# Kernel tuning notes

Measured on AMD Instinct MI355X. Metric: run time of the kernel, lower is better.

Reference implementation:

```python
import jax, jax.numpy as jnp
import numpy as np

B, S, T, E = 16, 512, 128, 256
VIN, VOUT, ENC, DEC = 32000, 32000, 32, 128


def pos_encoding(length, depth):
    # standard sinusoidal positional encoding (TF tutorial / AddPositionalEmbedding)
    half = depth // 2
    pos = jnp.arange(length, dtype=jnp.float32)[:, None]          # (L,1)
    rates = (1.0 / (10000.0 ** (jnp.arange(half, dtype=jnp.float32) / half)))[None, :]
    ang = pos * rates                                             # (L, depth/2)
    return jnp.concatenate([jnp.sin(ang), jnp.cos(ang)], axis=-1)  # (L, depth)


def lstm_scan(x, W, U, b, reverse=False):
    # Keras LSTM, gate order i,f,g,o; zero initial state. x: (B,S,E) -> (B,S,H), h_final
    Bn, H = x.shape[0], U.shape[0]
    def step(carry, xt):
        h, c = carry
        z = xt @ W + h @ U + b
        i, f, g, o = jnp.split(z, 4, axis=-1)
        c = jax.nn.sigmoid(f) * c + jax.nn.sigmoid(i) * jnp.tanh(g)
        h = jax.nn.sigmoid(o) * jnp.tanh(c)
        return (h, c), h
    h0 = jnp.zeros((Bn, H), x.dtype)
    (h, _), hs = jax.lax.scan(step, (h0, h0), jnp.swapaxes(x, 0, 1), reverse=reverse)
    return jnp.swapaxes(hs, 0, 1), h


def setup_inputs() -> dict:
    key = jax.random.key(0)
    ks = jax.random.split(key, 20)
    s = 0.05
    return {
        'source': jax.random.randint(ks[0], (B, S), 0, VIN, dtype=jnp.int32),
        'target': jax.random.randint(ks[1], (B, T), 0, VOUT, dtype=jnp.int32),
        'src_emb': jax.random.normal(ks[2], (VIN, E), jnp.float32) * s,
        'tgt_emb': jax.random.normal(ks[3], (VOUT, E), jnp.float32) * s,
        'Wf': jax.random.normal(ks[4], (E, 4 * ENC), jnp.float32) * s,
        'Uf': jax.random.normal(ks[5], (ENC, 4 * ENC), jnp.float32) * s,
        'bf': jnp.zeros((4 * ENC,), jnp.float32),
        'Wb': jax.random.normal(ks[6], (E, 4 * ENC), jnp.float32) * s,
        'Ub': jax.random.normal(ks[7], (ENC, 4 * ENC), jnp.float32) * s,
        'bb': jnp.zeros((4 * ENC,), jnp.float32),
        'W1': jax.random.normal(ks[8], (2 * ENC, DEC), jnp.float32) * s,
        'b1': jnp.zeros((DEC,), jnp.float32),
        'W2': jax.random.normal(ks[9], (2 * ENC, DEC), jnp.float32) * s,
        'b2': jnp.zeros((DEC,), jnp.float32),
        'Vw': jax.random.normal(ks[10], (DEC, 1), jnp.float32) * s,
        'Vb': jnp.zeros((1,), jnp.float32),
        'Wd': jax.random.normal(ks[11], (2 * ENC + E, 4 * DEC), jnp.float32) * s,
        'bd': jnp.zeros((4 * DEC,), jnp.float32),
        'Wfc': jax.random.normal(ks[12], (DEC, VOUT), jnp.float32) * s,
        'bfc': jnp.zeros((VOUT,), jnp.float32),
    }


def reference(source, target, src_emb, tgt_emb, Wf, Uf, bf, Wb, Ub, bb,
              W1, b1, W2, b2, Vw, Vb, Wd, bd, Wfc, bfc):
    # source embedding + positional encoding
    src = src_emb[source] * jnp.sqrt(jnp.float32(E)) + pos_encoding(S, E)  # (B,S,E)
    # bidirectional encoder (enc_units=32 each direction)
    out_f, hf = lstm_scan(src, Wf, Uf, bf)
    out_b, hb = lstm_scan(src, Wb, Ub, bb, reverse=True)
    enc = jnp.concatenate([out_f, out_b], axis=-1)        # (B,S,64)
    hidden = jnp.concatenate([hf, hb], axis=-1)           # (B,64) — constant query
    # Bahdanau attention with constant query -> constant context vector
    score = jnp.tanh(hidden[:, None, :] @ W1 + b1 + enc @ W2 + b2) @ Vw + Vb  # (B,S,1)
    attw = jax.nn.softmax(score, axis=1)
    ctx = jnp.sum(attw * enc, axis=1)                     # (B,64)
    # per-timestep decoder: LSTM restarts from zero state each step, so all
    # T steps are independent -> vectorize single LSTM step over T
    temb = tgt_emb[target]                                # (B,T,E)
    x = jnp.concatenate(
        [jnp.broadcast_to(ctx[:, None, :], (B, T, 2 * ENC)), temb], axis=-1)  # (B,T,320)
    z = x @ Wd + bd
    i, f, g, o = jnp.split(z, 4, axis=-1)
    c = jax.nn.sigmoid(i) * jnp.tanh(g)                   # c_prev = 0 => forget gate inert
    h = jax.nn.sigmoid(o) * jnp.tanh(c)                   # (B,T,128)
    return h @ Wfc + bfc                                  # (B,T,VOUT)
```

## Files before the change

kernel.cpp:

```cpp
#include <hip/hip_runtime.h>
#include <hip/hip_bf16.h>
#include <math.h>

#define BB 16
#define SS 512
#define TT 128
#define EE 256
#define ENC 32
#define DEC 128
#define VOUT 32000

typedef _Float16 half8 __attribute__((ext_vector_type(8)));
typedef float floatx4 __attribute__((ext_vector_type(4)));

__device__ __forceinline__ float sigmoidf_(float x) { return 1.0f / (1.0f + expf(-x)); }
__device__ __forceinline__ float rcpf_(float x) { return __builtin_amdgcn_rcpf(x); }

__global__ __launch_bounds__(256) void k_embed_gemm(
    const int* __restrict__ source, const float* __restrict__ src_emb,
    const float* __restrict__ Wf, const float* __restrict__ bf,
    const float* __restrict__ Wb, const float* __restrict__ bb,
    float* __restrict__ Zf, float* __restrict__ Zb)
{
    __shared__ __align__(16) float sSrc[8][EE];
    const int r0 = blockIdx.x * 8;
    const int tid = threadIdx.x;

    for (int idx = tid; idx < 8 * EE; idx += 256) {
        const int r = idx >> 8, e = idx & 255;
        const int row = r0 + r;
        const int s = row & (SS - 1);
        const int tok = source[row];
        float v = src_emb[(size_t)tok * EE + e] * 16.0f;
        const int jh = (e < 128) ? e : (e - 128);
        const float rate = expf(-0.07195578415f * (float)jh);
        const float ang = (float)s * rate;
        v += (e < 128) ? sinf(ang) : cosf(ang);
        sSrc[r][e] = v;
    }
    __syncthreads();

    const int j = tid & 127;
    const float* W = (tid < 128) ? Wf : Wb;
    const float* bv = (tid < 128) ? bf : bb;
    float* Zo = (tid < 128) ? Zf : Zb;

    float acc[8];
    const float bias = bv[j];
#pragma unroll
    for (int r = 0; r < 8; ++r) acc[r] = bias;

    for (int e = 0; e < EE; e += 4) {
        const float w0 = W[(e + 0) * 128 + j];
        const float w1 = W[(e + 1) * 128 + j];
        const float w2 = W[(e + 2) * 128 + j];
        const float w3 = W[(e + 3) * 128 + j];
#pragma unroll
        for (int r = 0; r < 8; ++r) {
            const float4 x = *(const float4*)&sSrc[r][e];
            acc[r] = fmaf(x.x, w0, acc[r]);
            acc[r] = fmaf(x.y, w1, acc[r]);
            acc[r] = fmaf(x.z, w2, acc[r]);
            acc[r] = fmaf(x.w, w3, acc[r]);
        }
    }
#pragma unroll
    for (int r = 0; r < 8; ++r) Zo[(size_t)(r0 + r) * 128 + j] = acc[r];
}

__global__ __launch_bounds__(64) void k_scan(
    const float* __restrict__ Zf, const float* __restrict__ Zb,
    const float* __restrict__ Uf, const float* __restrict__ Ub,
    float* __restrict__ enc, float* __restrict__ hidden)
{
    const int blk = blockIdx.x;
    const int batch = blk >> 1;
    const int dir = blk & 1;
    const float* __restrict__ Z = dir ? Zb : Zf;
    const float* __restrict__ U = dir ? Ub : Uf;
    const int lane = threadIdx.x;
    const int u = lane & 31;
    const int half = lane >> 5;
    const int colA = half * 64 + u;
    const int colB = half * 64 + 32 + u;

    float uA[ENC], uB[ENC];
#pragma unroll
    for (int k = 0; k < ENC; ++k) {
        uA[k] = U[k * 128 + colA];
        uB[k] = U[k * 128 + colB];
    }

    const float* __restrict__ Zrow = Z + (size_t)batch * (SS * 128);
    const int dt = dir ? -1 : 1;
    int t = dir ? (SS - 1) : 0;
    float zA = Zrow[t * 128 + colA];
    float zB = Zrow[t * 128 + colB];

    const float m = half ? 2.0f : 1.0f;
    const float madd = 1.0f - m;

    float h = 0.0f, c = 0.0f;

    for (int step = 0; step < SS; ++step) {
        float accA0 = zA, accA1 = 0.f, accA2 = 0.f, accA3 = 0.f;
        float accB0 = zB, accB1 = 0.f, accB2 = 0.f, accB3 = 0.f;
        if (step < SS - 1) {
            const int tn = t + dt;
            zA = Zrow[tn * 128 + colA];
            zB = Zrow[tn * 128 + colB];
        }
#pragma unroll
        for (int k = 0; k < ENC; k += 4) {
            const float h0 = __builtin_bit_cast(float,
                __builtin_amdgcn_readlane(__builtin_bit_cast(int, h), k + 0));
            const float h1 = __builtin_bit_cast(float,
                __builtin_amdgcn_readlane(__builtin_bit_cast(int, h), k + 1));
            const float h2 = __builtin_bit_cast(float,
                __builtin_amdgcn_readlane(__builtin_bit_cast(int, h), k + 2));
            const float h3 = __builtin_bit_cast(float,
                __builtin_amdgcn_readlane(__builtin_bit_cast(int, h), k + 3));
            accA0 = fmaf(h0, uA[k + 0], accA0);
            accB0 = fmaf(h0, uB[k + 0], accB0);
            accA1 = fmaf(h1, uA[k + 1], accA1);
            accB1 = fmaf(h1, uB[k + 1], accB1);
            accA2 = fmaf(h2, uA[k + 2], accA2);
            accB2 = fmaf(h2, uB[k + 2], accB2);
            accA3 = fmaf(h3, uA[k + 3], accA3);
            accB3 = fmaf(h3, uB[k + 3], accB3);
        }
        const float zAv = (accA0 + accA1) + (accA2 + accA3);
        const float zBv = (accB0 + accB1) + (accB2 + accB3);

        const float s1 = rcpf_(1.0f + expf(-m * zAv));
        const float a1 = fmaf(s1, m, madd);
        const float a2 = rcpf_(1.0f + expf(-zBv));

        const float t1 = __shfl_xor(a1, 32);
        const float t2 = __shfl_xor(a2, 32);

        c = fmaf(a2, c, a1 * t1);
        const float e2 = expf(-2.0f * c);
        const float tc = (1.0f - e2) * rcpf_(1.0f + e2);
        h = t2 * tc;

        if (half == 0)
            enc[((size_t)batch * SS + t) * 64 + dir * ENC + u] = h;
        t += dt;
    }
    if (half == 0)
        hidden[batch * 64 + dir * ENC + u] = h;
}

__global__ __launch_bounds__(128) void k_q(
    const float* __restrict__ hidden, const float* __restrict__ W1,
    const float* __restrict__ b1, const float* __restrict__ b2,
    float* __restrict__ q2)
{
    const int b = blockIdx.x, d = threadIdx.x;
    __shared__ __align__(16) float shid[64];
    if (d < 64) shid[d] = hidden[b * 64 + d];
    __syncthreads();
    float acc = b1[d] + b2[d];
#pragma unroll
    for (int k = 0; k < 64; k += 4) {
        const float4 h4 = *(const float4*)&shid[k];
        acc = fmaf(h4.x, W1[(k + 0) * 128 + d], acc);
        acc = fmaf(h4.y, W1[(k + 1) * 128 + d], acc);
        acc = fmaf(h4.z, W1[(k + 2) * 128 + d], acc);
        acc = fmaf(h4.w, W1[(k + 3) * 128 + d], acc);
    }
    q2[b * 128 + d] = acc;
}

__global__ __launch_bounds__(128) void k_score(
    const float* __restrict__ enc, const float* __restrict__ q2,
    const float* __restrict__ W2, const float* __restrict__ Vw,
    const float* __restrict__ Vb, float* __restrict__ scores)
{
    const int bs = blockIdx.x;
    const int b = bs >> 9;
    const int tid = threadIdx.x;
    __shared__ __align__(16) float se[64];
    __shared__ float sred2[2];
    if (tid < 64) se[tid] = enc[(size_t)bs * 64 + tid];
    __syncthreads();
    float acc = q2[b * 128 + tid];
#pragma unroll
    for (int k = 0; k < 64; k += 4) {
        const float4 e4 = *(const float4*)&se[k];
        acc = fmaf(e4.x, W2[(k + 0) * 128 + tid], acc);
        acc = fmaf(e4.y, W2[(k + 1) * 128 + tid], acc);
        acc = fmaf(e4.z, W2[(k + 2) * 128 + tid], acc);
        acc = fmaf(e4.w, W2[(k + 3) * 128 + tid], acc);
    }
    float v = tanhf(acc) * Vw[tid];
#pragma unroll
    for (int off = 32; off > 0; off >>= 1) v += __shfl_down(v, off);
    if ((tid & 63) == 0) sred2[tid >> 6] = v;
    __syncthreads();
    if (tid == 0) scores[bs] = sred2[0] + sred2[1] + Vb[0];
}

__global__ __launch_bounds__(512) void k_softmax_ctx(
    const float* __restrict__ scores, const float* __restrict__ enc,
    float* __restrict__ ctx)
{
    const int b = blockIdx.x, tid = threadIdx.x;
    __shared__ float sw[SS];
    __shared__ float sred[SS];
    const float sc = scores[b * SS + tid];
    sred[tid] = sc;
    __syncthreads();
    for (int s2 = 256; s2 > 0; s2 >>= 1) {
        if (tid < s2) sred[tid] = fmaxf(sred[tid], sred[tid + s2]);
        __syncthreads();
    }
    const float mx = sred[0];
    __syncthreads();
    const float ex = expf(sc - mx);
    sw[tid] = ex;
    sred[tid] = ex;
    __syncthreads();
    for (int s2 = 256; s2 > 0; s2 >>= 1) {
        if (tid < s2) sred[tid] += sred[tid + s2];
        __syncthreads();
    }
    const float inv = 1.0f / sred[0];
    __syncthreads();
    const int d = tid & 63, chunk = tid >> 6;
    float acc = 0.0f;
    const int sbeg = chunk * 64;
    for (int s = sbeg; s < sbeg + 64; ++s)
        acc = fmaf(sw[s], enc[((size_t)b * SS + s) * 64 + d], acc);
    sred[tid] = acc * inv;
    __syncthreads();
    if (tid < 64) {
        float t = 0.0f;
#pragma unroll
        for (int c = 0; c < 8; ++c) t += sred[c * 64 + tid];
        ctx[b * 64 + tid] = t;
    }
}

__global__ __launch_bounds__(384) void k_dec(
    const int* __restrict__ target, const float* __restrict__ tgt_emb,
    const float* __restrict__ ctx, const float* __restrict__ Wd,
    const float* __restrict__ bd, unsigned short* __restrict__ Ah)
{
    const int bt0 = blockIdx.x * 8;
    const int tid = threadIdx.x;
    __shared__ __align__(16) float sx[8][320];
    __shared__ float sg[3][8][128];

    for (int idx = tid; idx < 8 * 320; idx += 384) {
        const int r = idx / 320, k = idx % 320;
        const int bt = bt0 + r;
        const int b = bt >> 7;
        float v;
        if (k < 64) v = ctx[b * 64 + k];
        else v = tgt_emb[(size_t)target[bt] * EE + (k - 64)];
        sx[r][k] = v;
    }
    __syncthreads();

    const int g = tid >> 7, u = tid & 127;
    const int col = (g == 0) ? u : ((g == 1) ? (256 + u) : (384 + u));
    float acc[8];
    const float bias = bd[col];
#pragma unroll
    for (int r = 0; r < 8; ++r) acc[r] = bias;

#pragma unroll 2
    for (int k = 0; k < 320; k += 4) {
        const float w0 = Wd[(k + 0) * 512 + col];
        const float w1 = Wd[(k + 1) * 512 + col];
        const float w2 = Wd[(k + 2) * 512 + col];
        const float w3 = Wd[(k + 3) * 512 + col];
#pragma unroll
        for (int r = 0; r < 8; ++r) {
            const float4 x = *(const float4*)&sx[r][k];
            acc[r] = fmaf(x.x, w0, acc[r]);
            acc[r] = fmaf(x.y, w1, acc[r]);
            acc[r] = fmaf(x.z, w2, acc[r]);
            acc[r] = fmaf(x.w, w3, acc[r]);
        }
    }
#pragma unroll
    for (int r = 0; r < 8; ++r) {
        const float a = acc[r];
        sg[g][r][u] = (g == 1) ? tanhf(a) : sigmoidf_(a);
    }
    __syncthreads();
    if (tid < 128) {
#pragma unroll
        for (int r = 0; r < 8; ++r) {
            const float i_ = sg[0][r][u];
            const float g_ = sg[1][r][u];
            const float o_ = sg[2][r][u];
            const float h = o_ * tanhf(i_ * g_);
            Ah[(size_t)(bt0 + r) * 128 + u] =
                __builtin_bit_cast(unsigned short, (_Float16)h);
        }
    }
}

__global__ __launch_bounds__(256) void k_cvtB(
    const float* __restrict__ Wfc, unsigned short* __restrict__ Bt)
{
    __shared__ __align__(16) unsigned short sH[64][136];
    const int n0 = blockIdx.x * 64;
    const int tid = threadIdx.x;
    const int kk = tid >> 4;
    const int n4 = tid & 15;

#pragma unroll
    for (int p = 0; p < 8; ++p) {
        const int k = p * 16 + kk;
        const float4 v = *(const float4*)&Wfc[(size_t)k * VOUT + n0 + n4 * 4];
        sH[n4 * 4 + 0][k] = __builtin_bit_cast(unsigned short, (_Float16)v.x);
        sH[n4 * 4 + 1][k] = __builtin_bit_cast(unsigned short, (_Float16)v.y);
        sH[n4 * 4 + 2][k] = __builtin_bit_cast(unsigned short, (_Float16)v.z);
        sH[n4 * 4 + 3][k] = __builtin_bit_cast(unsigned short, (_Float16)v.w);
    }
    __syncthreads();

    const int r0 = tid >> 4;
    const int l8 = (tid & 15) * 8;
#pragma unroll
    for (int p = 0; p < 4; ++p) {
        const int r = p * 16 + r0;
        *(uint4*)&Bt[(size_t)(n0 + r) * 128 + l8] = *(const uint4*)&sH[r][l8];
    }
}

__global__ __launch_bounds__(256) void k_out_f16(
    const unsigned short* __restrict__ Ah,
    const unsigned short* __restrict__ Bt,
    const float* __restrict__ bias, float* __restrict__ C)
{
    const int tid  = threadIdx.x;
    const int wave = tid >> 6;
    const int lane = tid & 63;
    const int wm = wave >> 1, wn = wave & 1;
    const int rb = blockIdx.y * 128 + wm * 64;
    const int cb = blockIdx.x * 128 + wn * 64;
    const int lm = lane & 15;
    const int quad = lane >> 4;

    floatx4 acc[4][4];
#pragma unroll
    for (int nt = 0; nt < 4; ++nt) {
        const float bv = bias[cb + nt * 16 + lm];
#pragma unroll
        for (int mt = 0; mt < 4; ++mt)
            acc[mt][nt] = (floatx4){bv, bv, bv, bv};
    }

    const unsigned short* pA = Ah + (size_t)(rb + lm) * 128 + quad * 8;
    const unsigned short* pB = Bt + (size_t)(cb + lm) * 128 + quad * 8;

#pragma unroll
    for (int kc = 0; kc < 128; kc += 32) {
        half8 af[4], bfr[4];
#pragma unroll
        for (int mt = 0; mt < 4; ++mt)
            af[mt] = *(const half8*)(pA + mt * (16 * 128) + kc);
#pragma unroll
        for (int nt = 0; nt < 4; ++nt)
            bfr[nt] = *(const half8*)(pB + nt * (16 * 128) + kc);
#pragma unroll
        for (int mt = 0; mt < 4; ++mt)
#pragma unroll
            for (int nt = 0; nt < 4; ++nt)
                acc[mt][nt] = __builtin_amdgcn_mfma_f32_16x16x32_f16(
                    af[mt], bfr[nt], acc[mt][nt], 0, 0, 0);
    }

#pragma unroll
    for (int mt = 0; mt < 4; ++mt) {
        const int r0 = rb + mt * 16 + quad * 4;
#pragma unroll
        for (int nt = 0; nt < 4; ++nt) {
            const int col = cb + nt * 16 + lm;
            float* Cp = C + (size_t)r0 * VOUT + col;
#pragma unroll
            for (int r = 0; r < 4; ++r)
                Cp[(size_t)r * VOUT] = acc[mt][nt][r];
        }
    }
}

extern "C" void kernel_launch(void* const* d_in, const int* in_sizes, int n_in,
                              void* d_out, int out_size, void* d_ws, size_t ws_size,
                              hipStream_t stream) {
    (void)in_sizes; (void)n_in; (void)out_size; (void)ws_size;
    const int*   source  = (const int*)  d_in[0];
    const int*   target  = (const int*)  d_in[1];
    const float* src_emb = (const float*)d_in[2];
    const float* tgt_emb = (const float*)d_in[3];
    const float* Wf      = (const float*)d_in[4];
    const float* Uf      = (const float*)d_in[5];
    const float* bf      = (const float*)d_in[6];
    const float* Wb      = (const float*)d_in[7];
    const float* Ub      = (const float*)d_in[8];
    const float* bb      = (const float*)d_in[9];
    const float* W1      = (const float*)d_in[10];
    const float* b1      = (const float*)d_in[11];
    const float* W2      = (const float*)d_in[12];
    const float* b2      = (const float*)d_in[13];
    const float* Vw      = (const float*)d_in[14];
    const float* Vb      = (const float*)d_in[15];
    const float* Wd      = (const float*)d_in[16];
    const float* bd      = (const float*)d_in[17];
    const float* Wfc     = (const float*)d_in[18];
    const float* bfc     = (const float*)d_in[19];
    float* out = (float*)d_out;

    float* ws     = (float*)d_ws;
    float* Zf     = ws;
    float* Zb     = Zf + 1048576;
    float* enc    = Zb + 1048576;
    float* hidden = enc + 524288;
    float* q2     = hidden + 1024;
    float* scores = q2 + 2048;
    float* ctx    = scores + 8192;
    unsigned short* Ah = (unsigned short*)(ctx + 1024);
    unsigned short* Bt = (unsigned short*)Zf;

    k_embed_gemm<<<1024, 256, 0, stream>>>(source, src_emb, Wf, bf, Wb, bb, Zf, Zb);
    k_scan<<<32, 64, 0, stream>>>(Zf, Zb, Uf, Ub, enc, hidden);
    k_q<<<16, 128, 0, stream>>>(hidden, W1, b1, b2, q2);
    k_score<<<8192, 128, 0, stream>>>(enc, q2, W2, Vw, Vb, scores);
    k_softmax_ctx<<<16, 512, 0, stream>>>(scores, enc, ctx);
    k_cvtB<<<500, 256, 0, stream>>>(Wfc, Bt);
    k_dec<<<256, 384, 0, stream>>>(target, tgt_emb, ctx, Wd, bd, Ah);
    k_out_f16<<<dim3(250, 16), 256, 0, stream>>>(Ah, Bt, bfc, out);
}
```

Before: 641.9 us.

## Interleave LSTM gate columns, prefetch Z four steps ahead, use exp2 intrinsics

The embedding GEMM now writes its output with a column permutation, so each scan lane can fetch both of its gate pre-activations with a single float2 load. The recurrent scan loop is unrolled by four, with a rolling four-deep register prefetch of Z to hide global-load latency on the serial recurrence. expf calls are replaced by hardware exp2 with a log2(e) prescale to shorten each step's dependency chain. The prefetch reads up to four rows past the end of the sequence; those values are never used, but the reads can fall outside the buffer for the edge batches.

```diff
diff --git a/kernel.cpp b/kernel.cpp
--- a/kernel.cpp
+++ b/kernel.cpp
@@ -15,6 +15,8 @@
 
 __device__ __forceinline__ float sigmoidf_(float x) { return 1.0f / (1.0f + expf(-x)); }
 __device__ __forceinline__ float rcpf_(float x) { return __builtin_amdgcn_rcpf(x); }
+
+#define LOG2E 1.4426950408889634f
 
 __global__ __launch_bounds__(256) void k_embed_gemm(
     const int* __restrict__ source, const float* __restrict__ src_emb,
@@ -64,8 +66,9 @@
             acc[r] = fmaf(x.w, w3, acc[r]);
         }
     }
-#pragma unroll
-    for (int r = 0; r < 8; ++r) Zo[(size_t)(r0 + r) * 128 + j] = acc[r];
+    const int jperm = ((j >> 6) << 6) | ((j & 31) << 1) | ((j >> 5) & 1);
+#pragma unroll
+    for (int r = 0; r < 8; ++r) Zo[(size_t)(r0 + r) * 128 + jperm] = acc[r];
 }
 
 __global__ __launch_bounds__(64) void k_scan(
@@ -91,63 +94,77 @@
         uB[k] = U[k * 128 + colB];
     }
 
-    const float* __restrict__ Zrow = Z + (size_t)batch * (SS * 128);
     const int dt = dir ? -1 : 1;
-    int t = dir ? (SS - 1) : 0;
-    float zA = Zrow[t * 128 + colA];
-    float zB = Zrow[t * 128 + colB];
+    const int t0 = dir ? (SS - 1) : 0;
+    const int dstep = dt * 128;
+    const float* __restrict__ Zbase = Z + (size_t)batch * (SS * 128) + 2 * lane;
+    int zoff = t0 * 128;
+
+    float2 z0 = *(const float2*)(Zbase + zoff);
+    float2 z1 = *(const float2*)(Zbase + zoff + dstep);
+    float2 z2 = *(const float2*)(Zbase + zoff + 2 * dstep);
+    float2 z3 = *(const float2*)(Zbase + zoff + 3 * dstep);
+
+    float* __restrict__ ep = enc + ((size_t)batch * SS + t0) * 64 + dir * ENC + u;
+    const int estep = dt * 64;
 
     const float m = half ? 2.0f : 1.0f;
-    const float madd = 1.0f - m;
+    const float madd = half ? -1.0f : 0.0f;
+    const float mk = -LOG2E * m;
 
     float h = 0.0f, c = 0.0f;
 
-    for (int step = 0; step < SS; ++step) {
-        float accA0 = zA, accA1 = 0.f, accA2 = 0.f, accA3 = 0.f;
-        float accB0 = zB, accB1 = 0.f, accB2 = 0.f, accB3 = 0.f;
-        if (step < SS - 1) {
-            const int tn = t + dt;
-            zA = Zrow[tn * 128 + colA];
-            zB = Zrow[tn * 128 + colB];
-        }
-#pragma unroll
-        for (int k = 0; k < ENC; k += 4) {
-            const float h0 = __builtin_bit_cast(float,
-                __builtin_amdgcn_readlane(__builtin_bit_cast(int, h), k + 0));
-            const float h1 = __builtin_bit_cast(float,
-                __builtin_amdgcn_readlane(__builtin_bit_cast(int, h), k + 1));
-            const float h2 = __builtin_bit_cast(float,
-                __builtin_amdgcn_readlane(__builtin_bit_cast(int, h), k + 2));
-            const float h3 = __builtin_bit_cast(float,
-                __builtin_amdgcn_readlane(__builtin_bit_cast(int, h), k + 3));
-            accA0 = fmaf(h0, uA[k + 0], accA0);
-            accB0 = fmaf(h0, uB[k + 0], accB0);
-            accA1 = fmaf(h1, uA[k + 1], accA1);
-            accB1 = fmaf(h1, uB[k + 1], accB1);
-            accA2 = fmaf(h2, uA[k + 2], accA2);
-            accB2 = fmaf(h2, uB[k + 2], accB2);
-            accA3 = fmaf(h3, uA[k + 3], accA3);
-            accB3 = fmaf(h3, uB[k + 3], accB3);
-        }
-        const float zAv = (accA0 + accA1) + (accA2 + accA3);
-        const float zBv = (accB0 + accB1) + (accB2 + accB3);
-
-        const float s1 = rcpf_(1.0f + expf(-m * zAv));
-        const float a1 = fmaf(s1, m, madd);
-        const float a2 = rcpf_(1.0f + expf(-zBv));
-
-        const float t1 = __shfl_xor(a1, 32);
-        const float t2 = __shfl_xor(a2, 32);
-
-        c = fmaf(a2, c, a1 * t1);
-        const float e2 = expf(-2.0f * c);
-        const float tc = (1.0f - e2) * rcpf_(1.0f + e2);
-        h = t2 * tc;
-
-        if (half == 0)
-            enc[((size_t)batch * SS + t) * 64 + dir * ENC + u] = h;
-        t += dt;
-    }
+#define LSTM_STEP(ZS)                                                          \
+    do {                                                                       \
+        float accA0 = ZS.x, accA1 = 0.f, accA2 = 0.f, accA3 = 0.f;             \
+        float accB0 = ZS.y, accB1 = 0.f, accB2 = 0.f, accB3 = 0.f;             \
+        ZS = *(const float2*)(Zbase + zoff + 4 * dstep);     \
+        _Pragma("unroll")                                                      \
+        for (int k = 0; k < ENC; k += 4) {                                     \
+            const float h0 = __builtin_bit_cast(float,                         \
+                __builtin_amdgcn_readlane(__builtin_bit_cast(int, h), k + 0)); \
+            const float h1 = __builtin_bit_cast(float,                         \
+                __builtin_amdgcn_readlane(__builtin_bit_cast(int, h), k + 1)); \
+            const float h2 = __builtin_bit_cast(float,                         \
+                __builtin_amdgcn_readlane(__builtin_bit_cast(int, h), k + 2)); \
+            const float h3 = __builtin_bit_cast(float,                         \
+                __builtin_amdgcn_readlane(__builtin_bit_cast(int, h), k + 3)); \
+            accA0 = fmaf(h0, uA[k + 0], accA0);                                \
+            accB0 = fmaf(h0, uB[k + 0], accB0);                                \
+            accA1 = fmaf(h1, uA[k + 1], accA1);                                \
+            accB1 = fmaf(h1, uB[k + 1], accB1);                                \
+            accA2 = fmaf(h2, uA[k + 2], accA2);                                \
+            accB2 = fmaf(h2, uB[k + 2], accB2);                                \
+            accA3 = fmaf(h3, uA[k + 3], accA3);                                \
+            accB3 = fmaf(h3, uB[k + 3], accB3);                                \
+        }                                                                      \
+        const float zAv = (accA0 + accA1) + (accA2 + accA3);                   \
+        const float zBv = (accB0 + accB1) + (accB2 + accB3);                   \
+             \
+        const float s1 = rcpf_(1.0f + __builtin_amdgcn_exp2f(mk * zAv));       \
+        const float a1 = fmaf(s1, m, madd);                                    \
+        const float a2 = rcpf_(1.0f + __builtin_amdgcn_exp2f(-LOG2E * zBv));   \
+           \
+        const float t1 = __shfl_xor(a1, 32);                                   \
+        const float t2 = __shfl_xor(a2, 32);                                   \
+                    \
+        c = fmaf(a2, c, a1 * t1);                                              \
+        const float e2 = __builtin_amdgcn_exp2f(-2.0f * LOG2E * c);            \
+        const float tc = (1.0f - e2) * rcpf_(1.0f + e2);                       \
+        h = t2 * tc;                            \
+        if (half == 0) *ep = h;                                                \
+        ep += estep;                                                           \
+        zoff += dstep;                                                         \
+    } while (0)
+
+    for (int grp = 0; grp < SS / 4; ++grp) {
+        LSTM_STEP(z0);
+        LSTM_STEP(z1);
+        LSTM_STEP(z2);
+        LSTM_STEP(z3);
+    }
+#undef LSTM_STEP
+
     if (half == 0)
         hidden[batch * 64 + dir * ENC + u] = h;
 }
```

Measured after the change: 633.5 us. Within noise of the previous version (-1.3%).
